# Performance work log

Measured on AMD Instinct MI355X. Metric: run time of the kernel, lower is better.

The kernel has to match this reference:

```python
import jax, jax.numpy as jnp
import numpy as np

V, E, H, B, T = 50257, 1024, 1024, 64, 512  # vocab, embed, hidden, batch, steps
PADDING_TOKEN = 0


def setup_inputs() -> dict:
    key = jax.random.key(0)
    ks = jax.random.split(key, 6)
    s = 0.02
    emb = jax.random.normal(ks[0], (V, E), jnp.float32) * s
    emb = emb.at[PADDING_TOKEN].set(0.0)  # padding_idx row is zero
    W_ih = jax.random.normal(ks[1], (4 * H, E), jnp.float32) * s   # torch LSTMCell weight_ih
    W_hh = jax.random.normal(ks[2], (4 * H, H), jnp.float32) * s   # torch LSTMCell weight_hh
    W_cls = jax.random.normal(ks[3], (V, H), jnp.float32) * s      # classifier weight [out,in]
    b_cls = jnp.zeros((V,), jnp.float32)                            # classifier bias
    batch_reviews = jax.random.randint(ks[4], (B, T), 0, V)
    return dict(batch_reviews=batch_reviews, emb=emb, W_ih=W_ih, W_hh=W_hh,
                W_cls=W_cls, b_cls=b_cls)


def _lstm_scan(x_tbe, W_ih, W_hh):
    # torch.nn.LSTMCell math (bias=False); gate order: i, f, g, o
    Bn = x_tbe.shape[1]
    Hn = W_hh.shape[1]

    def cell(carry, x_be):
        h, c = carry
        gates = x_be @ W_ih.T + h @ W_hh.T              # [B, 4H]
        i, f, g, o = jnp.split(gates, 4, axis=-1)
        c2 = jax.nn.sigmoid(f) * c + jax.nn.sigmoid(i) * jnp.tanh(g)
        h2 = jax.nn.sigmoid(o) * jnp.tanh(c2)
        return (h2, c2), None

    init = (jnp.zeros((Bn, Hn), x_tbe.dtype), jnp.zeros((Bn, Hn), x_tbe.dtype))
    (h, c), _ = jax.lax.scan(cell, init, x_tbe)
    return h, c


def reference(batch_reviews, emb, W_ih, W_hh, W_cls, b_cls):
    x = emb[batch_reviews]               # [B, T, E] embedding lookup
    x_tbe = jnp.transpose(x, (1, 0, 2))  # [T, B, E] for time-major scan
    h, c = _lstm_scan(x_tbe, W_ih, W_hh) # final (h, c) state only
    logits = h @ W_cls.T + b_cls         # [B, V]
    return logits, h, c
```

## Files before the change

### kernel.cpp

```cpp
#include <hip/hip_runtime.h>

#define Bn 64
#define Tn 512
#define En 1024
#define Hn 1024
#define Vn 50257
#define CHUNK 64
#define NCHUNK (Tn / CHUNK)
#define AGENT __HIP_MEMORY_SCOPE_AGENT

typedef __attribute__((ext_vector_type(8))) short short8;
typedef __attribute__((ext_vector_type(4))) float f32x4;
typedef __attribute__((ext_vector_type(4))) unsigned int u32x4;

__device__ __forceinline__ unsigned short f2bf(float f) {
    union { float f; unsigned u; } x; x.f = f;
    unsigned r = x.u + 0x7FFFu + ((x.u >> 16) & 1u);
    return (unsigned short)(r >> 16);
}
__device__ __forceinline__ float bf2f(unsigned short u) {
    union { unsigned u; float f; } x; x.u = ((unsigned)u) << 16; return x.f;
}
__device__ __forceinline__ float sigm(float x) { return 1.0f / (1.0f + __expf(-x)); }
__device__ __forceinline__ float tanh_fast(float x) {
    float e = __expf(2.0f * x);
    return (e - 1.0f) / (e + 1.0f);
}

#define LDH(dst, base, IMM)                                                  \
    asm volatile("global_load_dwordx4 %0, %1, off offset:" #IMM " sc0 sc1"   \
                 : "=v"(dst) : "v"(base) : "memory")
#define VMW(N) do { asm volatile("s_waitcnt vmcnt(" #N ")" ::: "memory");    \
                    __builtin_amdgcn_sched_barrier(0); } while (0)
#define ISSUE_GRP(buf, O0, O1, O2, O3)                                       \
    do {                                                                     \
        LDH((buf)[0], ap0, O0); LDH((buf)[1], ap0, O1);                      \
        LDH((buf)[2], ap0, O2); LDH((buf)[3], ap0, O3);                      \
        LDH((buf)[4], ap1, O0); LDH((buf)[5], ap1, O1);                      \
        LDH((buf)[6], ap1, O2); LDH((buf)[7], ap1, O3);                      \
    } while (0)
#define MFMA_GRP(buf, jb)                                                    \
    do {                                                                     \
        _Pragma("unroll")                                                    \
        for (int jj = 0; jj < 4; ++jj) {                                     \
            union { u32x4 u; short8 s; } f0, f1;                             \
            f0.u = (buf)[jj]; f1.u = (buf)[4 + jj];                          \
            acc[0][0] = __builtin_amdgcn_mfma_f32_16x16x32_bf16(f0.s, breg[0][(jb) + jj], acc[0][0], 0, 0, 0); \
            acc[0][1] = __builtin_amdgcn_mfma_f32_16x16x32_bf16(f0.s, breg[1][(jb) + jj], acc[0][1], 0, 0, 0); \
            acc[1][0] = __builtin_amdgcn_mfma_f32_16x16x32_bf16(f1.s, breg[0][(jb) + jj], acc[1][0], 0, 0, 0); \
            acc[1][1] = __builtin_amdgcn_mfma_f32_16x16x32_bf16(f1.s, breg[1][(jb) + jj], acc[1][1], 0, 0, 0); \
        }                                                                    \
    } while (0)

__global__ __launch_bounds__(256)
void cvt_f32_bf16(const float* __restrict__ src, unsigned short* __restrict__ dst, int n4) {
    int i = blockIdx.x * 256 + threadIdx.x;
    if (i < n4) {
        float4 v = reinterpret_cast<const float4*>(src)[i];
        ushort4 o;
        o.x = f2bf(v.x); o.y = f2bf(v.y); o.z = f2bf(v.z); o.w = f2bf(v.w);
        reinterpret_cast<ushort4*>(dst)[i] = o;
    }
}

__global__ __launch_bounds__(256)
void gather_x(const int* __restrict__ tokens, const float* __restrict__ emb,
              unsigned short* __restrict__ X, int t0) {
    const int r = blockIdx.x;
    const int trel = r >> 6, b = r & 63;
    const int tok = tokens[b * Tn + t0 + trel];
    const float* src = emb + (size_t)tok * En;
    const int k = threadIdx.x * 4;
    float4 v = *reinterpret_cast<const float4*>(src + k);
    ushort4 o;
    o.x = f2bf(v.x); o.y = f2bf(v.y); o.z = f2bf(v.z); o.w = f2bf(v.w);
    *reinterpret_cast<ushort4*>(X + (size_t)r * En + k) = o;
}

__device__ __forceinline__ void gemm_tile(
    const unsigned short* __restrict__ X, const unsigned short* __restrict__ Wih,
    unsigned short* __restrict__ G, int bx, int by,
    unsigned short (*As)[72], unsigned short (*Bs)[72], int tid)
{
    const int w = tid >> 6, l = tid & 63;
    const int wr = w >> 1, wc = w & 1;
    const int koff = (l >> 4) * 8;

    f32x4 acc[4][4];
#pragma unroll
    for (int i = 0; i < 4; ++i)
#pragma unroll
        for (int j = 0; j < 4; ++j) acc[i][j] = (f32x4){0.f, 0.f, 0.f, 0.f};

    for (int kk = 0; kk < En / 64; ++kk) {
        __syncthreads();
#pragma unroll
        for (int j = 0; j < 4; ++j) {
            const int u = tid * 4 + j;
            const int row = u >> 3, ku = (u & 7) * 8;
            *reinterpret_cast<short8*>(&As[row][ku]) =
                *reinterpret_cast<const short8*>(X + (size_t)(by * 128 + row) * En + kk * 64 + ku);
            *reinterpret_cast<short8*>(&Bs[row][ku]) =
                *reinterpret_cast<const short8*>(Wih + (size_t)(bx * 128 + row) * En + kk * 64 + ku);
        }
        __syncthreads();

#pragma unroll
        for (int kc = 0; kc < 2; ++kc) {
            const int k0 = kc * 32 + koff;
            short8 af[4], bf[4];
#pragma unroll
            for (int i = 0; i < 4; ++i)
                af[i] = *reinterpret_cast<const short8*>(&As[wr * 64 + i * 16 + (l & 15)][k0]);
#pragma unroll
            for (int j = 0; j < 4; ++j)
                bf[j] = *reinterpret_cast<const short8*>(&Bs[wc * 64 + j * 16 + (l & 15)][k0]);
#pragma unroll
            for (int i = 0; i < 4; ++i)
#pragma unroll
                for (int j = 0; j < 4; ++j)
                    acc[i][j] = __builtin_amdgcn_mfma_f32_16x16x32_bf16(af[i], bf[j], acc[i][j], 0, 0, 0);
        }
    }

    const int rr = 4 * (l >> 4);
#pragma unroll
    for (int i = 0; i < 4; ++i) {
        const int row = by * 128 + wr * 64 + i * 16 + rr;
#pragma unroll
        for (int j = 0; j < 4; ++j) {
            const int col = bx * 128 + wc * 64 + j * 16 + (l & 15);
#pragma unroll
            for (int r = 0; r < 4; ++r)
                G[(size_t)(row + r) * 4096 + col] = f2bf(acc[i][j][r]);
        }
    }
}

__global__ __launch_bounds__(256)
void gemm_gin(const unsigned short* __restrict__ X, const unsigned short* __restrict__ Wih,
              unsigned short* __restrict__ G) {
    __shared__ __align__(16) unsigned short As[128][72];
    __shared__ __align__(16) unsigned short Bs[128][72];
    gemm_tile(X, Wih, G, blockIdx.x & 31, blockIdx.x >> 5, As, Bs, threadIdx.x);
}

__global__ __launch_bounds__(256, 1)
void lstm_fused(const unsigned short* __restrict__ Gcur, unsigned short* __restrict__ Gnext,
                const unsigned short* __restrict__ Xnext, const unsigned short* __restrict__ Wih,
                const unsigned short* __restrict__ Whh,
                unsigned short* __restrict__ h0, unsigned short* __restrict__ h1,
                float* __restrict__ c_state, unsigned* __restrict__ flags, int t0, int do_gemm,
                float* __restrict__ out_h, float* __restrict__ out_c)
{
    __shared__ __align__(16) char smem[2 * 128 * 72 * 2];

    const int tid = threadIdx.x;

    if (blockIdx.x >= 128) {
        if (!do_gemm) return;
        unsigned short (*As)[72] = reinterpret_cast<unsigned short(*)[72]>(smem);
        unsigned short (*Bs)[72] = reinterpret_cast<unsigned short(*)[72]>(smem + 128 * 72 * 2);
        const int base = (blockIdx.x - 128) * 8;
        for (int tt = 0; tt < 8; ++tt) {
            const int tile = base + tt;
            gemm_tile(Xnext, Wih, Gnext, tile & 31, tile >> 5, As, Bs, tid);
        }
        return;
    }

    typedef float RedT[2][2][64][4];
    RedT* red = reinterpret_cast<RedT*>(smem);

    const int b = blockIdx.x;
    const int w = tid >> 6, l = tid & 63;
    const int kh = w & 1, rh = w >> 1;
    const int koff = (l >> 4) * 8;
    const int lc = l & 15;
    const int hcol = b * 8 + (l & 7);

    short8 breg[2][16];
#pragma unroll
    for (int ct = 0; ct < 2; ++ct) {
        const int gate = ct * 2 + (lc >> 3);
        const unsigned short* wrow = Whh + ((size_t)gate * Hn + (b * 8 + (lc & 7))) * Hn;
#pragma unroll
        for (int j = 0; j < 16; ++j)
            breg[ct][j] = *reinterpret_cast<const short8*>(wrow + (kh * 16 + j) * 32 + koff);
    }

    float c_reg[2][4];
    if (kh == 0) {
#pragma unroll
        for (int rt = 0; rt < 2; ++rt)
#pragma unroll
            for (int r = 0; r < 4; ++r)
                c_reg[rt][r] = c_state[(rh * 32 + rt * 16 + ((l >> 4) << 2) + r) * Hn + hcol];
    }

    const int sg = lc >> 3;
    const int gc0 = sg * Hn + hcol;
    const int gc1 = (2 + sg) * Hn + hcol;

    unsigned short gp0[2][4], gp1[2][4];
    if (kh == 0) {
#pragma unroll
        for (int rt = 0; rt < 2; ++rt) {
            const int rowbase = rh * 32 + rt * 16 + ((l >> 4) << 2);
#pragma unroll
            for (int r = 0; r < 4; ++r) {
                gp0[rt][r] = Gcur[(size_t)(rowbase + r) * 4096 + gc0];
                gp1[rt][r] = Gcur[(size_t)(rowbase + r) * 4096 + gc1];
            }
        }
    }

    const unsigned* myflag = &flags[(kh * 64 + l) * 32];

    for (int s = 0; s < CHUNK; ++s) {
        const int t = t0 + s;
        const unsigned short* hin = (t & 1) ? h1 : h0;
        unsigned short* hout = (t & 1) ? h0 : h1;

        {
            const unsigned target = (unsigned)t;
            int guard = 0;
            while (__hip_atomic_load(myflag, __ATOMIC_RELAXED, AGENT) < target &&
                   guard < (1 << 16)) {
                __builtin_amdgcn_s_sleep(1);
                ++guard;
            }
        }
        __builtin_amdgcn_sched_barrier(0);

        const unsigned short* ap0 =
            hin + (size_t)(rh * 32 + (l & 15)) * Hn + kh * 512 + koff;
        const unsigned short* ap1 =
            hin + (size_t)(rh * 32 + 16 + (l & 15)) * Hn + kh * 512 + koff;

        f32x4 acc[2][2];
        acc[0][0] = acc[0][1] = acc[1][0] = acc[1][1] = (f32x4){0.f, 0.f, 0.f, 0.f};

        u32x4 bufA[8], bufB[8], bufC[8], bufD[8];
        ISSUE_GRP(bufA, 0,   64,  128, 192);
        ISSUE_GRP(bufB, 256, 320, 384, 448);
        ISSUE_GRP(bufC, 512, 576, 640, 704);
        ISSUE_GRP(bufD, 768, 832, 896, 960);

        VMW(24); MFMA_GRP(bufA, 0);
        VMW(16); MFMA_GRP(bufB, 4);
        VMW(8);  MFMA_GRP(bufC, 8);
        VMW(0);  MFMA_GRP(bufD, 12);

        if (kh == 1) {
#pragma unroll
            for (int rt = 0; rt < 2; ++rt)
#pragma unroll
                for (int ct = 0; ct < 2; ++ct)
                    *reinterpret_cast<f32x4*>(&red[rh][rt][ct][l][0]) = acc[rt][ct];
        }
        __syncthreads();

        if (kh == 0) {
#pragma unroll
            for (int rt = 0; rt < 2; ++rt) {
                const int rowbase = rh * 32 + rt * 16 + ((l >> 4) << 2);
                f32x4 a0 = acc[rt][0] + *reinterpret_cast<f32x4*>(&red[rh][rt][0][l][0]);
                f32x4 a1 = acc[rt][1] + *reinterpret_cast<f32x4*>(&red[rh][rt][1][l][0]);
#pragma unroll
                for (int r = 0; r < 4; ++r) {
                    float v0 = a0[r] + bf2f(gp0[rt][r]);
                    float v1 = a1[r] + bf2f(gp1[rt][r]);
                    float p0 = __shfl_xor(v0, 8);
                    float p1 = __shfl_xor(v1, 8);
                    float iv = (l & 8) ? p0 : v0;
                    float fv = (l & 8) ? v0 : p0;
                    float gv = (l & 8) ? p1 : v1;
                    float ov = (l & 8) ? v1 : p1;
                    float cn = sigm(fv) * c_reg[rt][r] + sigm(iv) * tanh_fast(gv);
                    float hn = sigm(ov) * tanh_fast(cn);
                    c_reg[rt][r] = cn;
                    unsigned hb = f2bf(hn);
                    unsigned partner = (unsigned)__shfl_xor((int)hb, 1);
                    if (!(l & 8) && !(l & 1)) {
                        unsigned val = (hb & 0xFFFFu) | (partner << 16);
                        __hip_atomic_store(
                            (unsigned*)(hout + (size_t)(rowbase + r) * Hn + hcol),
                            val, __ATOMIC_RELAXED, AGENT);
                    }
                    if (t == Tn - 1 && !(l & 8)) {
                        out_h[(rowbase + r) * Hn + hcol] = hn;
                        out_c[(rowbase + r) * Hn + hcol] = cn;
                    }
                }
            }
        }

        asm volatile("s_waitcnt vmcnt(0)" ::: "memory");
        __syncthreads();
        if (tid == 0)
            __hip_atomic_store(&flags[b * 32], (unsigned)(t + 1), __ATOMIC_RELAXED, AGENT);

        if (kh == 0 && s + 1 < CHUNK) {
            const unsigned short* Gt = Gcur + (size_t)(s + 1) * Bn * 4096;
#pragma unroll
            for (int rt = 0; rt < 2; ++rt) {
                const int rowbase = rh * 32 + rt * 16 + ((l >> 4) << 2);
#pragma unroll
                for (int r = 0; r < 4; ++r) {
                    gp0[rt][r] = Gt[(size_t)(rowbase + r) * 4096 + gc0];
                    gp1[rt][r] = Gt[(size_t)(rowbase + r) * 4096 + gc1];
                }
            }
        }
    }

    if (kh == 0 && !(l & 8)) {
#pragma unroll
        for (int rt = 0; rt < 2; ++rt)
#pragma unroll
            for (int r = 0; r < 4; ++r)
                c_state[(rh * 32 + rt * 16 + ((l >> 4) << 2) + r) * Hn + hcol] = c_reg[rt][r];
    }
}

__global__ __launch_bounds__(256)
void classifier(const unsigned short* __restrict__ h,
                const float* __restrict__ Wcls, const float* __restrict__ bcls,
                float* __restrict__ logits)
{
    __shared__ __align__(16) unsigned short Al[64][72];
    __shared__ __align__(16) unsigned short Bl[64][72];

    const int tid = threadIdx.x;
    const int v0 = blockIdx.x * 64;
    const int w = tid >> 6, l = tid & 63;
    const int lrow = tid >> 2, q = tid & 3;
    const int v = v0 + lrow;

    const unsigned short* hrow = h + lrow * Hn;
    const float* wrow = Wcls + (size_t)v * Hn;

    f32x4 acc[4];
#pragma unroll
    for (int ct = 0; ct < 4; ++ct) acc[ct] = (f32x4){0.f, 0.f, 0.f, 0.f};

    const int arow = w * 16 + (l & 15);
    const int koff = (l >> 4) * 8;

    for (int ch = 0; ch < 16; ++ch) {
        const int k0 = ch * 64;
        __syncthreads();
#pragma unroll
        for (int i2 = 0; i2 < 4; ++i2) {
            const int k = q * 4 + i2 * 16;
            *reinterpret_cast<ushort4*>(&Al[lrow][k]) =
                *reinterpret_cast<const ushort4*>(hrow + k0 + k);
            if (v < Vn) {
                float4 x = *reinterpret_cast<const float4*>(wrow + k0 + k);
                Bl[lrow][k + 0] = f2bf(x.x); Bl[lrow][k + 1] = f2bf(x.y);
                Bl[lrow][k + 2] = f2bf(x.z); Bl[lrow][k + 3] = f2bf(x.w);
            } else {
                ushort4 z; z.x = z.y = z.z = z.w = 0;
                *reinterpret_cast<ushort4*>(&Bl[lrow][k]) = z;
            }
        }
        __syncthreads();

        short8 a0 = *reinterpret_cast<const short8*>(&Al[arow][koff]);
        short8 a1 = *reinterpret_cast<const short8*>(&Al[arow][32 + koff]);
#pragma unroll
        for (int ct = 0; ct < 4; ++ct) {
            const int bcol = ct * 16 + (l & 15);
            short8 b0 = *reinterpret_cast<const short8*>(&Bl[bcol][koff]);
            short8 b1 = *reinterpret_cast<const short8*>(&Bl[bcol][32 + koff]);
            acc[ct] = __builtin_amdgcn_mfma_f32_16x16x32_bf16(a0, b0, acc[ct], 0, 0, 0);
            acc[ct] = __builtin_amdgcn_mfma_f32_16x16x32_bf16(a1, b1, acc[ct], 0, 0, 0);
        }
    }

    const int rr0 = w * 16 + (l >> 4) * 4;
#pragma unroll
    for (int ct = 0; ct < 4; ++ct) {
        const int vv = v0 + ct * 16 + (l & 15);
        if (vv < Vn) {
            float bb = bcls[vv];
#pragma unroll
            for (int r = 0; r < 4; ++r)
                logits[(size_t)(rr0 + r) * Vn + vv] = acc[ct][r] + bb;
        }
    }
}

extern "C" void kernel_launch(void* const* d_in, const int* in_sizes, int n_in,
                              void* d_out, int out_size, void* d_ws, size_t ws_size,
                              hipStream_t stream)
{
    const int*   tokens = (const int*)d_in[0];
    const float* emb    = (const float*)d_in[1];
    const float* W_ih   = (const float*)d_in[2];
    const float* W_hh   = (const float*)d_in[3];
    const float* W_cls  = (const float*)d_in[4];
    const float* b_cls  = (const float*)d_in[5];
    float* out = (float*)d_out;

    char* ws = (char*)d_ws;
    unsigned short* hbuf0 = (unsigned short*)ws;
    unsigned short* hbuf1 = (unsigned short*)(ws + 131072);
    float*          cst   = (float*)(ws + 262144);
    unsigned*       flags = (unsigned*)(ws + 524288);
    unsigned short* Wih_b = (unsigned short*)(ws + 540672);
    unsigned short* Whh_b = (unsigned short*)(ws + 540672 + 8388608);
    unsigned short* Xb    = (unsigned short*)(ws + 540672 + 2 * 8388608);
    unsigned short* Gb0   = (unsigned short*)(ws + 540672 + 3 * 8388608);
    unsigned short* Gb1   = (unsigned short*)(ws + 540672 + 3 * 8388608 + 33554432);

    hipMemsetAsync(ws, 0, 540672, stream);

    const int n4 = (4 * Hn * En) / 4;
    cvt_f32_bf16<<<n4 / 256, 256, 0, stream>>>(W_ih, Wih_b, n4);
    cvt_f32_bf16<<<n4 / 256, 256, 0, stream>>>(W_hh, Whh_b, n4);

    float* out_h = out + (size_t)Bn * Vn;
    float* out_c = out_h + Bn * Hn;

    gather_x<<<CHUNK * Bn, 256, 0, stream>>>(tokens, emb, Xb, 0);
    gemm_gin<<<32 * 32, 256, 0, stream>>>(Xb, Wih_b, Gb0);

    unsigned short* Gbuf[2] = {Gb0, Gb1};
    for (int c = 0; c < NCHUNK; ++c) {
        const int do_gemm = (c + 1 < NCHUNK) ? 1 : 0;
        if (do_gemm)
            gather_x<<<CHUNK * Bn, 256, 0, stream>>>(tokens, emb, Xb, (c + 1) * CHUNK);
        lstm_fused<<<256, 256, 0, stream>>>(Gbuf[c & 1], Gbuf[(c + 1) & 1], Xb,
                                            Wih_b, Whh_b, hbuf0, hbuf1,
                                            cst, flags, c * CHUNK, do_gemm,
                                            out_h, out_c);
    }

    classifier<<<(Vn + 63) / 64, 256, 0, stream>>>(hbuf0, W_cls, b_cls, out);
}
```

Baseline: 4.258 ms.

## Pack step flags and stage hidden state through LDS for coalesced stores

Result: slower. 5.444 ms (+27.9%).

```diff
diff --git a/kernel.cpp b/kernel.cpp
--- a/kernel.cpp
+++ b/kernel.cpp
@@ -30,6 +30,12 @@
 #define LDH(dst, base, IMM)                                                  \
     asm volatile("global_load_dwordx4 %0, %1, off offset:" #IMM " sc0 sc1"   \
                  : "=v"(dst) : "v"(base) : "memory")
+#define LDHA(dst, addr)                                                      \
+    asm volatile("global_load_dwordx4 %0, %1, off sc0 sc1"                   \
+                 : "=v"(dst) : "v"(addr) : "memory")
+#define STH(addr, data)                                                      \
+    asm volatile("global_store_dwordx4 %0, %1, off sc0 sc1"                  \
+                 :: "v"(addr), "v"(data) : "memory")
 #define VMW(N) do { asm volatile("s_waitcnt vmcnt(" #N ")" ::: "memory");    \
                     __builtin_amdgcn_sched_barrier(0); } while (0)
 #define ISSUE_GRP(buf, O0, O1, O2, O3)                                       \
@@ -171,6 +177,8 @@
 
     typedef float RedT[2][2][64][4];
     RedT* red = reinterpret_cast<RedT*>(smem);
+    unsigned short (*hl)[8] =
+        reinterpret_cast<unsigned short(*)[8]>(smem + 16384);
 
     const int b = blockIdx.x;
     const int w = tid >> 6, l = tid & 63;
@@ -215,23 +223,12 @@
         }
     }
 
-    const unsigned* myflag = &flags[(kh * 64 + l) * 32];
+    const char* fb = (const char*)flags + (l & 31) * 16;
 
     for (int s = 0; s < CHUNK; ++s) {
         const int t = t0 + s;
         const unsigned short* hin = (t & 1) ? h1 : h0;
         unsigned short* hout = (t & 1) ? h0 : h1;
-
-        {
-            const unsigned target = (unsigned)t;
-            int guard = 0;
-            while (__hip_atomic_load(myflag, __ATOMIC_RELAXED, AGENT) < target &&
-                   guard < (1 << 16)) {
-                __builtin_amdgcn_s_sleep(1);
-                ++guard;
-            }
-        }
-        __builtin_amdgcn_sched_barrier(0);
 
         const unsigned short* ap0 =
             hin + (size_t)(rh * 32 + (l & 15)) * Hn + kh * 512 + koff;
@@ -280,26 +277,26 @@
                     float cn = sigm(fv) * c_reg[rt][r] + sigm(iv) * tanh_fast(gv);
                     float hn = sigm(ov) * tanh_fast(cn);
                     c_reg[rt][r] = cn;
-                    unsigned hb = f2bf(hn);
-                    unsigned partner = (unsigned)__shfl_xor((int)hb, 1);
-                    if (!(l & 8) && !(l & 1)) {
-                        unsigned val = (hb & 0xFFFFu) | (partner << 16);
-                        __hip_atomic_store(
-                            (unsigned*)(hout + (size_t)(rowbase + r) * Hn + hcol),
-                            val, __ATOMIC_RELAXED, AGENT);
-                    }
-                    if (t == Tn - 1 && !(l & 8)) {
-                        out_h[(rowbase + r) * Hn + hcol] = hn;
-                        out_c[(rowbase + r) * Hn + hcol] = cn;
+                    if (!(l & 8)) {
+                        hl[rowbase + r][l & 7] = f2bf(hn);
+                        if (t == Tn - 1) {
+                            out_h[(rowbase + r) * Hn + hcol] = hn;
+                            out_c[(rowbase + r) * Hn + hcol] = cn;
+                        }
                     }
                 }
             }
         }
-
-        asm volatile("s_waitcnt vmcnt(0)" ::: "memory");
-        __syncthreads();
+        __syncthreads();
+
+        if (w == 0) {
+            u32x4 hv = *reinterpret_cast<const u32x4*>(&hl[l][0]);
+            const unsigned short* hp = hout + (size_t)l * Hn + b * 8;
+            STH(hp, hv);
+            asm volatile("s_waitcnt vmcnt(0)" ::: "memory");
+        }
         if (tid == 0)
-            __hip_atomic_store(&flags[b * 32], (unsigned)(t + 1), __ATOMIC_RELAXED, AGENT);
+            __hip_atomic_store(&flags[b], (unsigned)(t + 1), __ATOMIC_RELAXED, AGENT);
 
         if (kh == 0 && s + 1 < CHUNK) {
             const unsigned short* Gt = Gcur + (size_t)(s + 1) * Bn * 4096;
@@ -313,9 +310,25 @@
                 }
             }
         }
-    }
-
-    if (kh == 0 && !(l & 8)) {
+
+        {
+            const unsigned target = (unsigned)(t + 1);
+            int guard = 0;
+            while (guard < (1 << 16)) {
+                u32x4 fv;
+                LDHA(fv, fb);
+                asm volatile("s_waitcnt vmcnt(0)" ::: "memory");
+                __builtin_amdgcn_sched_barrier(0);
+                if (fv[0] >= target && fv[1] >= target &&
+                    fv[2] >= target && fv[3] >= target) break;
+                __builtin_amdgcn_s_sleep(1);
+                ++guard;
+            }
+        }
+        __builtin_amdgcn_sched_barrier(0);
+    }
+
+    if (kh == 0) {
 #pragma unroll
         for (int rt = 0; rt < 2; ++rt)
 #pragma unroll
```

## Triple-buffer hidden state and poll per-K-slice flags before issuing loads

Applied to the files above, without the earlier changes.

Measured after the change: 4.398 ms. 3.3% more time.

```diff
diff --git a/kernel.cpp b/kernel.cpp
--- a/kernel.cpp
+++ b/kernel.cpp
@@ -51,6 +51,19 @@
             acc[1][1] = __builtin_amdgcn_mfma_f32_16x16x32_bf16(f1.s, breg[1][(jb) + jj], acc[1][1], 0, 0, 0); \
         }                                                                    \
     } while (0)
+#define POLL16(pb, tgt)                                                      \
+    do {                                                                     \
+        unsigned fv_ = 0xFFFFFFFFu;                                          \
+        if (l < 16)                                                          \
+            fv_ = __hip_atomic_load(&flags[((pb) + l) * 32], __ATOMIC_RELAXED, AGENT); \
+        int g_ = 0;                                                          \
+        while (__any(fv_ < (unsigned)(tgt)) && g_ < (1 << 16)) {             \
+            __builtin_amdgcn_s_sleep(1);                                     \
+            if (l < 16)                                                      \
+                fv_ = __hip_atomic_load(&flags[((pb) + l) * 32], __ATOMIC_RELAXED, AGENT); \
+            ++g_;                                                            \
+        }                                                                    \
+    } while (0)
 
 __global__ __launch_bounds__(256)
 void cvt_f32_bf16(const float* __restrict__ src, unsigned short* __restrict__ dst, int n4) {
@@ -149,7 +162,8 @@
 void lstm_fused(const unsigned short* __restrict__ Gcur, unsigned short* __restrict__ Gnext,
                 const unsigned short* __restrict__ Xnext, const unsigned short* __restrict__ Wih,
                 const unsigned short* __restrict__ Whh,
-                unsigned short* __restrict__ h0, unsigned short* __restrict__ h1,
+                unsigned short* __restrict__ hb0, unsigned short* __restrict__ hb1,
+                unsigned short* __restrict__ hb2,
                 float* __restrict__ c_state, unsigned* __restrict__ flags, int t0, int do_gemm,
                 float* __restrict__ out_h, float* __restrict__ out_c)
 {
@@ -215,23 +229,12 @@
         }
     }
 
-    const unsigned* myflag = &flags[(kh * 64 + l) * 32];
+    const int pbase = kh * 64;
 
     for (int s = 0; s < CHUNK; ++s) {
         const int t = t0 + s;
-        const unsigned short* hin = (t & 1) ? h1 : h0;
-        unsigned short* hout = (t & 1) ? h0 : h1;
-
-        {
-            const unsigned target = (unsigned)t;
-            int guard = 0;
-            while (__hip_atomic_load(myflag, __ATOMIC_RELAXED, AGENT) < target &&
-                   guard < (1 << 16)) {
-                __builtin_amdgcn_s_sleep(1);
-                ++guard;
-            }
-        }
-        __builtin_amdgcn_sched_barrier(0);
+        const unsigned short* hin  = (t % 3 == 0) ? hb0 : ((t % 3 == 1) ? hb1 : hb2);
+        unsigned short*       hout = ((t + 1) % 3 == 0) ? hb0 : (((t + 1) % 3 == 1) ? hb1 : hb2);
 
         const unsigned short* ap0 =
             hin + (size_t)(rh * 32 + (l & 15)) * Hn + kh * 512 + koff;
@@ -242,10 +245,10 @@
         acc[0][0] = acc[0][1] = acc[1][0] = acc[1][1] = (f32x4){0.f, 0.f, 0.f, 0.f};
 
         u32x4 bufA[8], bufB[8], bufC[8], bufD[8];
-        ISSUE_GRP(bufA, 0,   64,  128, 192);
-        ISSUE_GRP(bufB, 256, 320, 384, 448);
-        ISSUE_GRP(bufC, 512, 576, 640, 704);
-        ISSUE_GRP(bufD, 768, 832, 896, 960);
+        POLL16(pbase + 0,  t); ISSUE_GRP(bufA, 0,   64,  128, 192);
+        POLL16(pbase + 16, t); ISSUE_GRP(bufB, 256, 320, 384, 448);
+        POLL16(pbase + 32, t); ISSUE_GRP(bufC, 512, 576, 640, 704);
+        POLL16(pbase + 48, t); ISSUE_GRP(bufD, 768, 832, 896, 960);
 
         VMW(24); MFMA_GRP(bufA, 0);
         VMW(16); MFMA_GRP(bufB, 4);
@@ -260,6 +263,19 @@
                     *reinterpret_cast<f32x4*>(&red[rh][rt][ct][l][0]) = acc[rt][ct];
         }
         __syncthreads();
+
+        if (t >= 2) {
+            const unsigned tgt2 = (unsigned)(t - 1);
+            unsigned fa = __hip_atomic_load(&flags[l * 32], __ATOMIC_RELAXED, AGENT);
+            unsigned fb = __hip_atomic_load(&flags[(64 + l) * 32], __ATOMIC_RELAXED, AGENT);
+            int guard = 0;
+            while (__any((fa < tgt2) || (fb < tgt2)) && guard < (1 << 16)) {
+                __builtin_amdgcn_s_sleep(1);
+                fa = __hip_atomic_load(&flags[l * 32], __ATOMIC_RELAXED, AGENT);
+                fb = __hip_atomic_load(&flags[(64 + l) * 32], __ATOMIC_RELAXED, AGENT);
+                ++guard;
+            }
+        }
 
         if (kh == 0) {
 #pragma unroll
@@ -407,15 +423,16 @@
     char* ws = (char*)d_ws;
     unsigned short* hbuf0 = (unsigned short*)ws;
     unsigned short* hbuf1 = (unsigned short*)(ws + 131072);
-    float*          cst   = (float*)(ws + 262144);
-    unsigned*       flags = (unsigned*)(ws + 524288);
-    unsigned short* Wih_b = (unsigned short*)(ws + 540672);
-    unsigned short* Whh_b = (unsigned short*)(ws + 540672 + 8388608);
-    unsigned short* Xb    = (unsigned short*)(ws + 540672 + 2 * 8388608);
-    unsigned short* Gb0   = (unsigned short*)(ws + 540672 + 3 * 8388608);
-    unsigned short* Gb1   = (unsigned short*)(ws + 540672 + 3 * 8388608 + 33554432);
-
-    hipMemsetAsync(ws, 0, 540672, stream);
+    unsigned short* hbuf2 = (unsigned short*)(ws + 262144);
+    float*          cst   = (float*)(ws + 393216);
+    unsigned*       flags = (unsigned*)(ws + 655360);
+    unsigned short* Wih_b = (unsigned short*)(ws + 671744);
+    unsigned short* Whh_b = (unsigned short*)(ws + 671744 + 8388608);
+    unsigned short* Xb    = (unsigned short*)(ws + 671744 + 2 * 8388608);
+    unsigned short* Gb0   = (unsigned short*)(ws + 671744 + 3 * 8388608);
+    unsigned short* Gb1   = (unsigned short*)(ws + 671744 + 3 * 8388608 + 33554432);
+
+    hipMemsetAsync(ws, 0, 671744, stream);
 
     const int n4 = (4 * Hn * En) / 4;
     cvt_f32_bf16<<<n4 / 256, 256, 0, stream>>>(W_ih, Wih_b, n4);
@@ -433,10 +450,10 @@
         if (do_gemm)
             gather_x<<<CHUNK * Bn, 256, 0, stream>>>(tokens, emb, Xb, (c + 1) * CHUNK);
         lstm_fused<<<256, 256, 0, stream>>>(Gbuf[c & 1], Gbuf[(c + 1) & 1], Xb,
-                                            Wih_b, Whh_b, hbuf0, hbuf1,
+                                            Wih_b, Whh_b, hbuf0, hbuf1, hbuf2,
                                             cst, flags, c * CHUNK, do_gemm,
                                             out_h, out_c);
     }
 
-    classifier<<<(Vn + 63) / 64, 256, 0, stream>>>(hbuf0, W_cls, b_cls, out);
-}
+    classifier<<<(Vn + 63) / 64, 256, 0, stream>>>(hbuf2, W_cls, b_cls, out);
+}
```

## Replace per-step flag spin with parity-tagged h values and triple buffering

Applied to the files above, without the earlier changes.

New measurement: 6.620 ms. 1.55x slower.

```diff
diff --git a/kernel.cpp b/kernel.cpp
--- a/kernel.cpp
+++ b/kernel.cpp
@@ -52,6 +52,27 @@
         }                                                                    \
     } while (0)
 
+__device__ __forceinline__ unsigned tagmask8(const u32x4* buf, unsigned expw) {
+    unsigned m = 0;
+#pragma unroll
+    for (int i = 0; i < 8; ++i) {
+        u32x4 v = buf[i];
+        m |= (v[0] ^ expw) | (v[1] ^ expw) | (v[2] ^ expw) | (v[3] ^ expw);
+    }
+    return m & 0x00010001u;
+}
+#define RETRY_GRP(buf, O0, O1, O2, O3)                                       \
+    do {                                                                     \
+        unsigned m_ = tagmask8(buf, expw);                                   \
+        int g_ = 0;                                                          \
+        while (__any(m_ != 0) && g_ < (1 << 14)) {                           \
+            ISSUE_GRP(buf, O0, O1, O2, O3);                                  \
+            VMW(0);                                                          \
+            m_ = tagmask8(buf, expw);                                        \
+            ++g_;                                                            \
+        }                                                                    \
+    } while (0)
+
 __global__ __launch_bounds__(256)
 void cvt_f32_bf16(const float* __restrict__ src, unsigned short* __restrict__ dst, int n4) {
     int i = blockIdx.x * 256 + threadIdx.x;
@@ -149,7 +170,8 @@
 void lstm_fused(const unsigned short* __restrict__ Gcur, unsigned short* __restrict__ Gnext,
                 const unsigned short* __restrict__ Xnext, const unsigned short* __restrict__ Wih,
                 const unsigned short* __restrict__ Whh,
-                unsigned short* __restrict__ h0, unsigned short* __restrict__ h1,
+                unsigned short* __restrict__ hb0, unsigned short* __restrict__ hb1,
+                unsigned short* __restrict__ hb2, unsigned short* __restrict__ hclean,
                 float* __restrict__ c_state, unsigned* __restrict__ flags, int t0, int do_gemm,
                 float* __restrict__ out_h, float* __restrict__ out_c)
 {
@@ -170,7 +192,6 @@
     }
 
     typedef float RedT[2][2][64][4];
-    RedT* red = reinterpret_cast<RedT*>(smem);
 
     const int b = blockIdx.x;
     const int w = tid >> 6, l = tid & 63;
@@ -215,23 +236,12 @@
         }
     }
 
-    const unsigned* myflag = &flags[(kh * 64 + l) * 32];
-
     for (int s = 0; s < CHUNK; ++s) {
         const int t = t0 + s;
-        const unsigned short* hin = (t & 1) ? h1 : h0;
-        unsigned short* hout = (t & 1) ? h0 : h1;
-
-        {
-            const unsigned target = (unsigned)t;
-            int guard = 0;
-            while (__hip_atomic_load(myflag, __ATOMIC_RELAXED, AGENT) < target &&
-                   guard < (1 << 16)) {
-                __builtin_amdgcn_s_sleep(1);
-                ++guard;
-            }
-        }
-        __builtin_amdgcn_sched_barrier(0);
+        const unsigned short* hin  = (t % 3 == 0) ? hb0 : ((t % 3 == 1) ? hb1 : hb2);
+        unsigned short*       hout = ((t + 1) % 3 == 0) ? hb0 : (((t + 1) % 3 == 1) ? hb1 : hb2);
+        const unsigned expw = (t & 1) ? 0x00010001u : 0u;
+        const unsigned tb   = (unsigned)((t + 1) & 1);
 
         const unsigned short* ap0 =
             hin + (size_t)(rh * 32 + (l & 15)) * Hn + kh * 512 + koff;
@@ -247,11 +257,12 @@
         ISSUE_GRP(bufC, 512, 576, 640, 704);
         ISSUE_GRP(bufD, 768, 832, 896, 960);
 
-        VMW(24); MFMA_GRP(bufA, 0);
-        VMW(16); MFMA_GRP(bufB, 4);
-        VMW(8);  MFMA_GRP(bufC, 8);
-        VMW(0);  MFMA_GRP(bufD, 12);
-
+        VMW(24); RETRY_GRP(bufA, 0,   64,  128, 192); MFMA_GRP(bufA, 0);
+        VMW(16); RETRY_GRP(bufB, 256, 320, 384, 448); MFMA_GRP(bufB, 4);
+        VMW(8);  RETRY_GRP(bufC, 512, 576, 640, 704); MFMA_GRP(bufC, 8);
+        VMW(0);  RETRY_GRP(bufD, 768, 832, 896, 960); MFMA_GRP(bufD, 12);
+
+        RedT* red = reinterpret_cast<RedT*>(smem + (t & 1) * 16384);
         if (kh == 1) {
 #pragma unroll
             for (int rt = 0; rt < 2; ++rt)
@@ -261,7 +272,23 @@
         }
         __syncthreads();
 
+        if (tid == 0)
+            __hip_atomic_store(&flags[b * 32], (unsigned)(t + 1), __ATOMIC_RELAXED, AGENT);
+
         if (kh == 0) {
+            if (t >= 2) {
+                const unsigned tgt2 = (unsigned)(t - 1);
+                unsigned fa = __hip_atomic_load(&flags[l * 32], __ATOMIC_RELAXED, AGENT);
+                unsigned fbv = __hip_atomic_load(&flags[(64 + l) * 32], __ATOMIC_RELAXED, AGENT);
+                int guard = 0;
+                while (__any((fa < tgt2) || (fbv < tgt2)) && guard < (1 << 16)) {
+                    __builtin_amdgcn_s_sleep(1);
+                    fa = __hip_atomic_load(&flags[l * 32], __ATOMIC_RELAXED, AGENT);
+                    fbv = __hip_atomic_load(&flags[(64 + l) * 32], __ATOMIC_RELAXED, AGENT);
+                    ++guard;
+                }
+            }
+
 #pragma unroll
             for (int rt = 0; rt < 2; ++rt) {
                 const int rowbase = rh * 32 + rt * 16 + ((l >> 4) << 2);
@@ -280,7 +307,7 @@
                     float cn = sigm(fv) * c_reg[rt][r] + sigm(iv) * tanh_fast(gv);
                     float hn = sigm(ov) * tanh_fast(cn);
                     c_reg[rt][r] = cn;
-                    unsigned hb = f2bf(hn);
+                    unsigned hb = ((unsigned)f2bf(hn) & 0xFFFEu) | tb;
                     unsigned partner = (unsigned)__shfl_xor((int)hb, 1);
                     if (!(l & 8) && !(l & 1)) {
                         unsigned val = (hb & 0xFFFFu) | (partner << 16);
@@ -291,25 +318,21 @@
                     if (t == Tn - 1 && !(l & 8)) {
                         out_h[(rowbase + r) * Hn + hcol] = hn;
                         out_c[(rowbase + r) * Hn + hcol] = cn;
+                        hclean[(rowbase + r) * Hn + hcol] = f2bf(hn);
                     }
                 }
             }
-        }
-
-        asm volatile("s_waitcnt vmcnt(0)" ::: "memory");
-        __syncthreads();
-        if (tid == 0)
-            __hip_atomic_store(&flags[b * 32], (unsigned)(t + 1), __ATOMIC_RELAXED, AGENT);
-
-        if (kh == 0 && s + 1 < CHUNK) {
-            const unsigned short* Gt = Gcur + (size_t)(s + 1) * Bn * 4096;
-#pragma unroll
-            for (int rt = 0; rt < 2; ++rt) {
-                const int rowbase = rh * 32 + rt * 16 + ((l >> 4) << 2);
-#pragma unroll
-                for (int r = 0; r < 4; ++r) {
-                    gp0[rt][r] = Gt[(size_t)(rowbase + r) * 4096 + gc0];
-                    gp1[rt][r] = Gt[(size_t)(rowbase + r) * 4096 + gc1];
+
+            if (s + 1 < CHUNK) {
+                const unsigned short* Gt = Gcur + (size_t)(s + 1) * Bn * 4096;
+#pragma unroll
+                for (int rt = 0; rt < 2; ++rt) {
+                    const int rowbase = rh * 32 + rt * 16 + ((l >> 4) << 2);
+#pragma unroll
+                    for (int r = 0; r < 4; ++r) {
+                        gp0[rt][r] = Gt[(size_t)(rowbase + r) * 4096 + gc0];
+                        gp1[rt][r] = Gt[(size_t)(rowbase + r) * 4096 + gc1];
+                    }
                 }
             }
         }
@@ -405,17 +428,21 @@
     float* out = (float*)d_out;
 
     char* ws = (char*)d_ws;
-    unsigned short* hbuf0 = (unsigned short*)ws;
-    unsigned short* hbuf1 = (unsigned short*)(ws + 131072);
-    float*          cst   = (float*)(ws + 262144);
-    unsigned*       flags = (unsigned*)(ws + 524288);
-    unsigned short* Wih_b = (unsigned short*)(ws + 540672);
-    unsigned short* Whh_b = (unsigned short*)(ws + 540672 + 8388608);
-    unsigned short* Xb    = (unsigned short*)(ws + 540672 + 2 * 8388608);
-    unsigned short* Gb0   = (unsigned short*)(ws + 540672 + 3 * 8388608);
-    unsigned short* Gb1   = (unsigned short*)(ws + 540672 + 3 * 8388608 + 33554432);
-
-    hipMemsetAsync(ws, 0, 540672, stream);
+    unsigned short* hbuf0  = (unsigned short*)ws;
+    unsigned short* hbuf1  = (unsigned short*)(ws + 131072);
+    unsigned short* hbuf2  = (unsigned short*)(ws + 262144);
+    unsigned short* hclean = (unsigned short*)(ws + 393216);
+    float*          cst    = (float*)(ws + 524288);
+    unsigned*       flags  = (unsigned*)(ws + 786432);
+    unsigned short* Wih_b  = (unsigned short*)(ws + 802816);
+    unsigned short* Whh_b  = (unsigned short*)(ws + 802816 + 8388608);
+    unsigned short* Xb     = (unsigned short*)(ws + 802816 + 2 * 8388608);
+    unsigned short* Gb0    = (unsigned short*)(ws + 802816 + 3 * 8388608);
+    unsigned short* Gb1    = (unsigned short*)(ws + 802816 + 3 * 8388608 + 33554432);
+
+    hipMemsetAsync(ws, 0, 262144, stream);
+    hipMemsetAsync(ws + 262144, 0x01, 131072, stream);
+    hipMemsetAsync(ws + 393216, 0, 409600, stream);
 
     const int n4 = (4 * Hn * En) / 4;
     cvt_f32_bf16<<<n4 / 256, 256, 0, stream>>>(W_ih, Wih_b, n4);
@@ -433,10 +460,10 @@
         if (do_gemm)
             gather_x<<<CHUNK * Bn, 256, 0, stream>>>(tokens, emb, Xb, (c + 1) * CHUNK);
         lstm_fused<<<256, 256, 0, stream>>>(Gbuf[c & 1], Gbuf[(c + 1) & 1], Xb,
-                                            Wih_b, Whh_b, hbuf0, hbuf1,
+                                            Wih_b, Whh_b, hbuf0, hbuf1, hbuf2, hclean,
                                             cst, flags, c * CHUNK, do_gemm,
                                             out_h, out_c);
     }
 
-    classifier<<<(Vn + 63) / 64, 256, 0, stream>>>(hbuf0, W_cls, b_cls, out);
-}
+    classifier<<<(Vn + 63) / 64, 256, 0, stream>>>(hclean, W_cls, b_cls, out);
+}
```
